# Optimization experiments

Hardware: AMD Instinct MI355X
Metric: run time of the kernel (lower is better)

The kernel has to match this reference:

```python
import jax, jax.numpy as jnp
import numpy as np

N = 50000   # nodes
D = 128     # hidden dim
E_NS = 250000  # non-self-loop edges
B = 4096    # sessions
NEG_SLOPE = 0.01  # F.leaky_relu default


def setup_inputs() -> dict:
    key = jax.random.key(0)
    ks = jax.random.split(key, 8)
    x = jax.random.normal(ks[0], (N, D), jnp.float32)
    src = jax.random.randint(ks[1], (E_NS,), 0, N)
    off = jax.random.randint(ks[2], (E_NS,), 1, N)
    dst = (src + off) % N  # guarantees src != dst
    loops = jnp.arange(N)
    edge_index = jnp.stack([jnp.concatenate([src, loops]),
                            jnp.concatenate([dst, loops])])  # [2, E_NS+N]
    batch = jnp.sort(jax.random.randint(ks[3], (N,), 0, B))
    local_sess_avg = jax.random.normal(ks[4], (B, D), jnp.float32)
    stdv = 1.0 / np.sqrt(D)
    W_alpha = jax.random.uniform(ks[5], (1, D), jnp.float32, -stdv, stdv)
    W_forward = jax.random.uniform(ks[6], (1, D), jnp.float32, -stdv, stdv)
    W_backward = jax.random.uniform(ks[7], (1, D), jnp.float32, -stdv, stdv)
    mt_sess_masks = jnp.ones((N,), jnp.int32)
    return {"x": x, "W_alpha": W_alpha, "W_forward": W_forward,
            "W_backward": W_backward, "local_sess_avg": local_sess_avg,
            "edge_index": edge_index, "batch": batch,
            "mt_sess_masks": mt_sess_masks, "n_nonself": E_NS}


def reference(x, W_alpha, W_forward, W_backward, local_sess_avg,
              edge_index, batch, mt_sess_masks, n_nonself):
    n = x.shape[0]
    src, dst = edge_index[0], edge_index[1]
    # non-self-loop edges occupy the first n_nonself columns (static int)
    src_ns, dst_ns = src[:n_nonself], dst[:n_nonself]
    # expanded edges = original edges + reversed non-self-loop edges
    exp_src = jnp.concatenate([src, dst_ns])  # [Et]
    exp_dst = jnp.concatenate([dst, src_ns])  # [Et]

    lrelu = lambda v: jax.nn.leaky_relu(v, NEG_SLOPE)

    exp_xi = x[exp_dst]                     # [Et, D]
    exp_xj = x[exp_src]                     # [Et, D]
    alpha_query = local_sess_avg[batch[exp_dst]]  # [Et, D]
    alpha = lrelu((exp_xi * alpha_query) @ W_alpha.T)        # [Et, 1]
    beta = lrelu((x[dst] * x[src]) @ W_forward.T)            # [E, 1]
    rbeta = lrelu((x[dst_ns] * x[src_ns]) @ W_backward.T)    # [E_ns, 1]
    logits = (jnp.concatenate([beta, rbeta], axis=0) + alpha)[:, 0]  # [Et]

    # segment softmax over target nodes (every node has a self-loop)
    seg_max = jax.lax.stop_gradient(
        jax.ops.segment_max(logits, exp_dst, num_segments=n))
    ex = jnp.exp(logits - seg_max[exp_dst])
    denom = jax.ops.segment_sum(ex, exp_dst, num_segments=n)
    aij = ex / denom[exp_dst]

    # scatter-add weighted neighbor features
    aggr = jax.ops.segment_sum(aij[:, None] * exp_xj, exp_dst, num_segments=n)

    # update: masked nodes take aggregate, others keep x; residual add
    new_x = jnp.where((mt_sess_masks == 1)[:, None], aggr, x)
    return new_x + x
```

## Files before the change

### kernel.cpp

```cpp
#include <hip/hip_runtime.h>

#define NEG_SLOPE 0.01f
#define STRIDE 48

__device__ __forceinline__ float lrelu(float v) { return v > 0.f ? v : NEG_SLOPE * v; }

__device__ __forceinline__ float dot4(float4 a, float4 b) {
    return a.x * b.x + a.y * b.y + a.z * b.z + a.w * b.w;
}

__device__ __forceinline__ void placeEdge(int s, int d, unsigned flag,
                                          int* __restrict__ cursor, int* __restrict__ slots) {
    int pos = atomicAdd(&cursor[d], 1);
    if (pos < STRIDE) slots[d * STRIDE + pos] = (int)((unsigned)s | flag);
}

__global__ void fill_kernel(const int* __restrict__ EI0, const int* __restrict__ EI1,
                            int* __restrict__ cursor, int* __restrict__ slots,
                            int E_total, int E_NS) {
    int t = blockIdx.x * blockDim.x + threadIdx.x;
    int n1v = E_total >> 2, n0v = E_NS >> 2;
    if (t < n1v) {
        int4 s = ((const int4*)EI0)[t];
        int4 d = ((const int4*)EI1)[t];
        placeEdge(s.x, d.x, 0u, cursor, slots);
        placeEdge(s.y, d.y, 0u, cursor, slots);
        placeEdge(s.z, d.z, 0u, cursor, slots);
        placeEdge(s.w, d.w, 0u, cursor, slots);
    } else if (t < n1v + n0v) {
        int u = t - n1v;
        int4 s = ((const int4*)EI1)[u];
        int4 d = ((const int4*)EI0)[u];
        placeEdge(s.x, d.x, 0x80000000u, cursor, slots);
        placeEdge(s.y, d.y, 0x80000000u, cursor, slots);
        placeEdge(s.z, d.z, 0x80000000u, cursor, slots);
        placeEdge(s.w, d.w, 0x80000000u, cursor, slots);
    } else if (t == n1v + n0v) {
        for (int e = E_total & ~3; e < E_total; e++)
            placeEdge(EI0[e], EI1[e], 0u, cursor, slots);
        for (int e = E_NS & ~3; e < E_NS; e++)
            placeEdge(EI1[e], EI0[e], 0x80000000u, cursor, slots);
    }
}

__global__ void __launch_bounds__(256) gather_kernel(
                              const float4* __restrict__ x4,
                              const float4* __restrict__ Wf4, const float4* __restrict__ Wb4,
                              const int* __restrict__ cursor, const int* __restrict__ slots,
                              const int* __restrict__ mask,
                              float4* __restrict__ out4, int N) {
    int tid = blockIdx.x * blockDim.x + threadIdx.x;
    int node = tid >> 4;
    int sub = threadIdx.x & 15;
    int lane = threadIdx.x & 63;
    int gbase = lane & 48;
    bool active = (node < N);
    int nodeSafe = active ? node : 0;

    long long base = (long long)nodeSafe * 32;
    float4 xda = x4[base + sub];
    float4 xdb = x4[base + 16 + sub];
    int msk = active ? mask[nodeSafe] : 0;
    int cnt = (active && msk == 1) ? min(cursor[nodeSafe], STRIDE) : 0;

    const int4* sb4 = (const int4*)(slots + (long long)nodeSafe * STRIDE);
    int4 myee = make_int4(0, 0, 0, 0);
    if (sub < 12) myee = sb4[sub];

    float4 wfa = Wf4[sub], wfb = Wf4[16 + sub];
    float4 wba = Wb4[sub], wbb = Wb4[16 + sub];
    float4 yfa = {xda.x * wfa.x, xda.y * wfa.y, xda.z * wfa.z, xda.w * wfa.w};
    float4 yfb = {xdb.x * wfb.x, xdb.y * wfb.y, xdb.z * wfb.z, xdb.w * wfb.w};
    float4 yba = {xda.x * wba.x, xda.y * wba.y, xda.z * wba.z, xda.w * wba.w};
    float4 ybb = {xdb.x * wbb.x, xdb.y * wbb.y, xdb.z * wbb.z, xdb.w * wbb.w};

    float l = 0.f;
    float4 Oa = {0.f, 0.f, 0.f, 0.f}, Ob = {0.f, 0.f, 0.f, 0.f};
    int Nm1 = N - 1;

    for (int i = 0; i < cnt; i += 4) {
        int srcLane = gbase | (i >> 2);
        int e0 = __shfl(myee.x, srcLane, 64);
        int e1 = __shfl(myee.y, srcLane, 64);
        int e2 = __shfl(myee.z, srcLane, 64);
        int e3 = __shfl(myee.w, srcLane, 64);
        bool v1 = (i + 1 < cnt), v2 = (i + 2 < cnt), v3 = (i + 3 < cnt);
        long long s0 = (long long)min(e0 & 0x7fffffff, Nm1) * 32;
        long long s1 = (long long)min(e1 & 0x7fffffff, Nm1) * 32;
        long long s2 = (long long)min(e2 & 0x7fffffff, Nm1) * 32;
        long long s3 = (long long)min(e3 & 0x7fffffff, Nm1) * 32;
        float4 r0a = x4[s0 + sub], r0b = x4[s0 + 16 + sub];
        float4 r1a = x4[s1 + sub], r1b = x4[s1 + 16 + sub];
        float4 r2a = x4[s2 + sub], r2b = x4[s2 + 16 + sub];
        float4 r3a = x4[s3 + sub], r3b = x4[s3 + 16 + sub];
        bool f0 = (e0 < 0), f1 = (e1 < 0), f2 = (e2 < 0), f3 = (e3 < 0);

        float p0 = dot4(r0a, f0 ? yba : yfa) + dot4(r0b, f0 ? ybb : yfb);
        float p1 = dot4(r1a, f1 ? yba : yfa) + dot4(r1b, f1 ? ybb : yfb);
        float p2 = dot4(r2a, f2 ? yba : yfa) + dot4(r2b, f2 ? ybb : yfb);
        float p3 = dot4(r3a, f3 ? yba : yfa) + dot4(r3b, f3 ? ybb : yfb);
#pragma unroll
        for (int sh = 1; sh < 16; sh <<= 1) {
            p0 += __shfl_xor(p0, sh, 64);
            p1 += __shfl_xor(p1, sh, 64);
            p2 += __shfl_xor(p2, sh, 64);
            p3 += __shfl_xor(p3, sh, 64);
        }

        float ev0 = __expf(lrelu(p0));
        float ev1 = v1 ? __expf(lrelu(p1)) : 0.f;
        float ev2 = v2 ? __expf(lrelu(p2)) : 0.f;
        float ev3 = v3 ? __expf(lrelu(p3)) : 0.f;
        l += ev0 + ev1 + ev2 + ev3;
        Oa.x += ev0 * r0a.x + ev1 * r1a.x + ev2 * r2a.x + ev3 * r3a.x;
        Oa.y += ev0 * r0a.y + ev1 * r1a.y + ev2 * r2a.y + ev3 * r3a.y;
        Oa.z += ev0 * r0a.z + ev1 * r1a.z + ev2 * r2a.z + ev3 * r3a.z;
        Oa.w += ev0 * r0a.w + ev1 * r1a.w + ev2 * r2a.w + ev3 * r3a.w;
        Ob.x += ev0 * r0b.x + ev1 * r1b.x + ev2 * r2b.x + ev3 * r3b.x;
        Ob.y += ev0 * r0b.y + ev1 * r1b.y + ev2 * r2b.y + ev3 * r3b.y;
        Ob.z += ev0 * r0b.z + ev1 * r1b.z + ev2 * r2b.z + ev3 * r3b.z;
        Ob.w += ev0 * r0b.w + ev1 * r1b.w + ev2 * r2b.w + ev3 * r3b.w;
    }

    if (active) {
        float4 ra, rb;
        if (msk == 1) {
            float inv = (l > 0.f) ? 1.f / l : 0.f;
            ra = {Oa.x * inv + xda.x, Oa.y * inv + xda.y, Oa.z * inv + xda.z, Oa.w * inv + xda.w};
            rb = {Ob.x * inv + xdb.x, Ob.y * inv + xdb.y, Ob.z * inv + xdb.z, Ob.w * inv + xdb.w};
        } else {
            ra = {2.f * xda.x, 2.f * xda.y, 2.f * xda.z, 2.f * xda.w};
            rb = {2.f * xdb.x, 2.f * xdb.y, 2.f * xdb.z, 2.f * xdb.w};
        }
        out4[base + sub] = ra;
        out4[base + 16 + sub] = rb;
    }
}

extern "C" void kernel_launch(void* const* d_in, const int* in_sizes, int n_in,
                              void* d_out, int out_size, void* d_ws, size_t ws_size,
                              hipStream_t stream) {
    const float* x   = (const float*)d_in[0];
    const float* Wf  = (const float*)d_in[2];
    const float* Wb  = (const float*)d_in[3];
    const int* EI    = (const int*)d_in[5];
    const int* mask  = (const int*)d_in[7];

    int N = in_sizes[6];
    int E_total = in_sizes[5] / 2;
    int E_NS = E_total - N;

    const int* EI0 = EI;
    const int* EI1 = EI + E_total;

    char* ws = (char*)d_ws;
    int* cursor = (int*)ws;
    int* slots  = (int*)(ws + (size_t)N * 4);

    hipMemsetAsync(cursor, 0, (size_t)N * 4, stream);

    const int BLK = 256;
    int edgeVecThreads = (E_total >> 2) + (E_NS >> 2) + 1;
    int edgeVecBlocks = (edgeVecThreads + BLK - 1) / BLK;
    int nodeBlocks = ((N * 16) + BLK - 1) / BLK;

    fill_kernel<<<edgeVecBlocks, BLK, 0, stream>>>(EI0, EI1, cursor, slots, E_total, E_NS);
    gather_kernel<<<nodeBlocks, BLK, 0, stream>>>(
        (const float4*)x, (const float4*)Wf, (const float4*)Wb,
        cursor, slots, mask, (float4*)d_out, N);
}
```

Before: 157.7 us.

## Fuse CSR build and gather into one cooperative kernel, handle self-loops implicitly

Replaces the memset, fill and gather launches with a single cooperative persistent kernel that zeroes counters, buckets edges, and aggregates, separated by grid-wide syncs. Self-loop edges are no longer inserted into slots; their contribution is computed directly from the node's own features, reducing atomics and slot usage. It falls back to the old multi-kernel path if cooperative launch fails. The cost is two grid syncs and fewer resident threads looping over nodes.

```diff
diff --git a/kernel.cpp b/kernel.cpp
--- a/kernel.cpp
+++ b/kernel.cpp
@@ -1,4 +1,7 @@
 #include <hip/hip_runtime.h>
+#include <hip/hip_cooperative_groups.h>
+
+namespace cg = cooperative_groups;
 
 #define NEG_SLOPE 0.01f
 #define STRIDE 48
@@ -13,6 +16,144 @@
                                           int* __restrict__ cursor, int* __restrict__ slots) {
     int pos = atomicAdd(&cursor[d], 1);
     if (pos < STRIDE) slots[d * STRIDE + pos] = (int)((unsigned)s | flag);
+}
+
+__global__ void __launch_bounds__(256) fused_kernel(
+        const float4* __restrict__ x4,
+        const float4* __restrict__ Wf4, const float4* __restrict__ Wb4,
+        const int* __restrict__ EI0, const int* __restrict__ EI1,
+        int* __restrict__ cursor, int* __restrict__ slots,
+        const int* __restrict__ mask,
+        float4* __restrict__ out4, int N, int E_NS) {
+    cg::grid_group grid = cg::this_grid();
+    int tid = blockIdx.x * blockDim.x + threadIdx.x;
+    int nthreads = gridDim.x * blockDim.x;
+
+    for (int i = tid; i < N; i += nthreads) cursor[i] = 0;
+
+    __threadfence();
+    grid.sync();
+
+    int n0v = E_NS >> 2;
+    for (int t = tid; t < 2 * n0v; t += nthreads) {
+        if (t < n0v) {
+            int4 s = ((const int4*)EI0)[t];
+            int4 d = ((const int4*)EI1)[t];
+            placeEdge(s.x, d.x, 0u, cursor, slots);
+            placeEdge(s.y, d.y, 0u, cursor, slots);
+            placeEdge(s.z, d.z, 0u, cursor, slots);
+            placeEdge(s.w, d.w, 0u, cursor, slots);
+        } else {
+            int u = t - n0v;
+            int4 s = ((const int4*)EI1)[u];
+            int4 d = ((const int4*)EI0)[u];
+            placeEdge(s.x, d.x, 0x80000000u, cursor, slots);
+            placeEdge(s.y, d.y, 0x80000000u, cursor, slots);
+            placeEdge(s.z, d.z, 0x80000000u, cursor, slots);
+            placeEdge(s.w, d.w, 0x80000000u, cursor, slots);
+        }
+    }
+    if (tid == 0) {
+        for (int e = E_NS & ~3; e < E_NS; e++) {
+            placeEdge(EI0[e], EI1[e], 0u, cursor, slots);
+            placeEdge(EI1[e], EI0[e], 0x80000000u, cursor, slots);
+        }
+    }
+
+    __threadfence();
+    grid.sync();
+    __threadfence();
+
+    int sub = threadIdx.x & 15;
+    int lane = threadIdx.x & 63;
+    int gbase = lane & 48;
+    int group = tid >> 4;
+    int ngroups = nthreads >> 4;
+    int Nm1 = N - 1;
+
+    float4 wfa = Wf4[sub], wfb = Wf4[16 + sub];
+    float4 wba = Wb4[sub], wbb = Wb4[16 + sub];
+
+    for (int node = group; node < N; node += ngroups) {
+        long long base = (long long)node * 32;
+        float4 xda = x4[base + sub];
+        float4 xdb = x4[base + 16 + sub];
+        int msk = mask[node];
+        int cnt = (msk == 1) ? min(cursor[node], STRIDE) : 0;
+
+        const int4* sb4 = (const int4*)(slots + (long long)node * STRIDE);
+        int4 myee = make_int4(0, 0, 0, 0);
+        if (sub < 12) myee = sb4[sub];
+
+        float4 yfa = {xda.x * wfa.x, xda.y * wfa.y, xda.z * wfa.z, xda.w * wfa.w};
+        float4 yfb = {xdb.x * wfb.x, xdb.y * wfb.y, xdb.z * wfb.z, xdb.w * wfb.w};
+        float4 yba = {xda.x * wba.x, xda.y * wba.y, xda.z * wba.z, xda.w * wba.w};
+        float4 ybb = {xdb.x * wbb.x, xdb.y * wbb.y, xdb.z * wbb.z, xdb.w * wbb.w};
+
+        float ps = dot4(xda, yfa) + dot4(xdb, yfb);
+#pragma unroll
+        for (int sh = 1; sh < 16; sh <<= 1) ps += __shfl_xor(ps, sh, 64);
+        float evs = __expf(lrelu(ps));
+        float l = evs;
+        float4 Oa = {evs * xda.x, evs * xda.y, evs * xda.z, evs * xda.w};
+        float4 Ob = {evs * xdb.x, evs * xdb.y, evs * xdb.z, evs * xdb.w};
+
+        for (int i = 0; i < cnt; i += 4) {
+            int srcLane = gbase | (i >> 2);
+            int e0 = __shfl(myee.x, srcLane, 64);
+            int e1 = __shfl(myee.y, srcLane, 64);
+            int e2 = __shfl(myee.z, srcLane, 64);
+            int e3 = __shfl(myee.w, srcLane, 64);
+            bool v1 = (i + 1 < cnt), v2 = (i + 2 < cnt), v3 = (i + 3 < cnt);
+            long long s0 = (long long)min(e0 & 0x7fffffff, Nm1) * 32;
+            long long s1 = (long long)min(e1 & 0x7fffffff, Nm1) * 32;
+            long long s2 = (long long)min(e2 & 0x7fffffff, Nm1) * 32;
+            long long s3 = (long long)min(e3 & 0x7fffffff, Nm1) * 32;
+            float4 r0a = x4[s0 + sub], r0b = x4[s0 + 16 + sub];
+            float4 r1a = x4[s1 + sub], r1b = x4[s1 + 16 + sub];
+            float4 r2a = x4[s2 + sub], r2b = x4[s2 + 16 + sub];
+            float4 r3a = x4[s3 + sub], r3b = x4[s3 + 16 + sub];
+            bool f0 = (e0 < 0), f1 = (e1 < 0), f2 = (e2 < 0), f3 = (e3 < 0);
+
+            float p0 = dot4(r0a, f0 ? yba : yfa) + dot4(r0b, f0 ? ybb : yfb);
+            float p1 = dot4(r1a, f1 ? yba : yfa) + dot4(r1b, f1 ? ybb : yfb);
+            float p2 = dot4(r2a, f2 ? yba : yfa) + dot4(r2b, f2 ? ybb : yfb);
+            float p3 = dot4(r3a, f3 ? yba : yfa) + dot4(r3b, f3 ? ybb : yfb);
+#pragma unroll
+            for (int sh = 1; sh < 16; sh <<= 1) {
+                p0 += __shfl_xor(p0, sh, 64);
+                p1 += __shfl_xor(p1, sh, 64);
+                p2 += __shfl_xor(p2, sh, 64);
+                p3 += __shfl_xor(p3, sh, 64);
+            }
+
+            float ev0 = __expf(lrelu(p0));
+            float ev1 = v1 ? __expf(lrelu(p1)) : 0.f;
+            float ev2 = v2 ? __expf(lrelu(p2)) : 0.f;
+            float ev3 = v3 ? __expf(lrelu(p3)) : 0.f;
+            l += ev0 + ev1 + ev2 + ev3;
+            Oa.x += ev0 * r0a.x + ev1 * r1a.x + ev2 * r2a.x + ev3 * r3a.x;
+            Oa.y += ev0 * r0a.y + ev1 * r1a.y + ev2 * r2a.y + ev3 * r3a.y;
+            Oa.z += ev0 * r0a.z + ev1 * r1a.z + ev2 * r2a.z + ev3 * r3a.z;
+            Oa.w += ev0 * r0a.w + ev1 * r1a.w + ev2 * r2a.w + ev3 * r3a.w;
+            Ob.x += ev0 * r0b.x + ev1 * r1b.x + ev2 * r2b.x + ev3 * r3b.x;
+            Ob.y += ev0 * r0b.y + ev1 * r1b.y + ev2 * r2b.y + ev3 * r3b.y;
+            Ob.z += ev0 * r0b.z + ev1 * r1b.z + ev2 * r2b.z + ev3 * r3b.z;
+            Ob.w += ev0 * r0b.w + ev1 * r1b.w + ev2 * r2b.w + ev3 * r3b.w;
+        }
+
+        float4 ra, rb;
+        if (msk == 1) {
+            float inv = (l > 0.f) ? 1.f / l : 0.f;
+            ra = {Oa.x * inv + xda.x, Oa.y * inv + xda.y, Oa.z * inv + xda.z, Oa.w * inv + xda.w};
+            rb = {Ob.x * inv + xdb.x, Ob.y * inv + xdb.y, Ob.z * inv + xdb.z, Ob.w * inv + xdb.w};
+        } else {
+            ra = {2.f * xda.x, 2.f * xda.y, 2.f * xda.z, 2.f * xda.w};
+            rb = {2.f * xdb.x, 2.f * xdb.y, 2.f * xdb.z, 2.f * xdb.w};
+        }
+        out4[base + sub] = ra;
+        out4[base + 16 + sub] = rb;
+    }
 }
 
 __global__ void fill_kernel(const int* __restrict__ EI0, const int* __restrict__ EI1,
@@ -157,15 +298,36 @@
     int* cursor = (int*)ws;
     int* slots  = (int*)(ws + (size_t)N * 4);
 
-    hipMemsetAsync(cursor, 0, (size_t)N * 4, stream);
-
     const int BLK = 256;
-    int edgeVecThreads = (E_total >> 2) + (E_NS >> 2) + 1;
-    int edgeVecBlocks = (edgeVecThreads + BLK - 1) / BLK;
-    int nodeBlocks = ((N * 16) + BLK - 1) / BLK;
-
-    fill_kernel<<<edgeVecBlocks, BLK, 0, stream>>>(EI0, EI1, cursor, slots, E_total, E_NS);
-    gather_kernel<<<nodeBlocks, BLK, 0, stream>>>(
-        (const float4*)x, (const float4*)Wf, (const float4*)Wb,
-        cursor, slots, mask, (float4*)d_out, N);
-}
+
+    static int coopBlocks = -2;
+    if (coopBlocks == -2) {
+        int perCU = 0;
+        hipError_t qe = hipOccupancyMaxActiveBlocksPerMultiprocessor(
+            &perCU, (const void*)fused_kernel, BLK, 0);
+        coopBlocks = (qe == hipSuccess && perCU > 0) ? perCU * 256 : -1;
+        if (coopBlocks > 4096) coopBlocks = 4096;
+    }
+
+    bool launched = false;
+    if (coopBlocks > 0) {
+        void* args[] = {(void*)&x, (void*)&Wf, (void*)&Wb, (void*)&EI0, (void*)&EI1,
+                        (void*)&cursor, (void*)&slots, (void*)&mask,
+                        (void*)&d_out, (void*)&N, (void*)&E_NS};
+        hipError_t err = hipLaunchCooperativeKernel(
+            (const void*)fused_kernel, dim3(coopBlocks), dim3(BLK), args, 0, stream);
+        launched = (err == hipSuccess);
+        if (!launched) coopBlocks = -1;
+    }
+
+    if (!launched) {
+        hipMemsetAsync(cursor, 0, (size_t)N * 4, stream);
+        int edgeVecThreads = (E_total >> 2) + (E_NS >> 2) + 1;
+        int edgeVecBlocks = (edgeVecThreads + BLK - 1) / BLK;
+        int nodeBlocks = ((N * 16) + BLK - 1) / BLK;
+        fill_kernel<<<edgeVecBlocks, BLK, 0, stream>>>(EI0, EI1, cursor, slots, E_total, E_NS);
+        gather_kernel<<<nodeBlocks, BLK, 0, stream>>>(
+            (const float4*)x, (const float4*)Wf, (const float4*)Wb,
+            cursor, slots, mask, (float4*)d_out, N);
+    }
+}
```

Measured after the change: 388.1 us. 2.46x slower.
